# Kernel tuning notes

Hardware: AMD Instinct MI355X
Metric: run time of the kernel (lower is better)

The kernel has to match this reference:

```python
import jax, jax.numpy as jnp
import numpy as np

SEQ, IN, H = 64, 100000, 50


def setup_inputs() -> dict:
    key = jax.random.key(0)
    k0, k1, k2, k3, k4 = jax.random.split(key, 5)
    x = jax.random.normal(k0, (SEQ, 1, IN), dtype=jnp.float32) * 0.02
    Wi = jax.random.normal(k1, (IN, 4 * H), dtype=jnp.float32) * 0.01
    bi = jax.random.normal(k2, (4 * H,), dtype=jnp.float32) * 0.01
    Wh = jax.random.normal(k3, (H, 4 * H), dtype=jnp.float32) * 0.1
    bh = jax.random.normal(k4, (4 * H,), dtype=jnp.float32) * 0.01
    return {"x": x, "Wi": Wi, "bi": bi, "Wh": Wh, "bh": bh}


def reference(x, Wi, bi, Wh, bh):
    # x: [seq, batch=1, input_size] -- each row is a flattened ParameterList.
    # Precompute the input projection for all steps at once (one big GEMM),
    # same math as per-step input_weights(input) since it has no recurrence.
    gates_in = jnp.einsum('sbi,ig->sbg', x, Wi) + bi + bh  # [seq, 1, 4H]

    def step(carry, g_in):
        hx, cx = carry
        gates = g_in + hx @ Wh  # [1, 4H]
        i, f, g, o = jnp.split(gates, 4, axis=1)
        i = jax.nn.sigmoid(i)
        f = jax.nn.sigmoid(f)
        g = jnp.tanh(g)
        o = jax.nn.sigmoid(o)
        cy = f * cx + i * g
        hy = o * jnp.tanh(cy)
        return (hy, cy), None

    h0 = jnp.zeros((1, H), dtype=x.dtype)
    c0 = jnp.zeros((1, H), dtype=x.dtype)
    (h_final, _), _ = jax.lax.scan(step, (h0, c0), gates_in)
    # torch.squeeze(out_hidden): (1, H) -> (H,)
    return jnp.squeeze(h_final)
```

## Files before the change

kernel.cpp:

```cpp
#include <hip/hip_runtime.h>
#include <hip/hip_bf16.h>


#define K_DIM 100000
#define NG 200
#define NS 64
#define TK 32
#define NBLK 512
#define KSTRIDE (NBLK * TK)
#define CELLS (NS * NG)

__global__ __launch_bounds__(512, 4) void k1_gemm_partial(
    const float* __restrict__ x, const float* __restrict__ Wi,
    float* __restrict__ partial)
{
    __shared__ float4 ws4[TK * 50 + 16];

    const int tid  = threadIdx.x;
    const int lane = tid & 63;
    const int wave = tid >> 6;
    const int s0u  = __builtin_amdgcn_readfirstlane(wave * 8);

    float4 acc4[8];
#pragma unroll
    for (int j = 0; j < 8; ++j) acc4[j] = make_float4(0.f, 0.f, 0.f, 0.f);

    int kt = blockIdx.x * TK;
    const float4* wi4 = (const float4*)Wi;

    float4 w0, w1, w2, w3 = make_float4(0.f, 0.f, 0.f, 0.f);
    {
        const float4* wt = wi4 + (size_t)kt * 50;
        w0 = wt[tid];
        w1 = wt[tid + 512];
        w2 = wt[tid + 1024];
        if (tid < 64) w3 = wt[tid + 1536];
    }

    for (; kt < K_DIM; kt += KSTRIDE) {
        __syncthreads();
        ws4[tid]        = w0;
        ws4[tid + 512]  = w1;
        ws4[tid + 1024] = w2;
        if (tid < 64) ws4[tid + 1536] = w3;
        __syncthreads();

        int ktn = kt + KSTRIDE;
        if (ktn < K_DIM) {
            const float4* wt = wi4 + (size_t)ktn * 50;
            w0 = wt[tid];
            w1 = wt[tid + 512];
            w2 = wt[tid + 1024];
            if (tid < 64) w3 = wt[tid + 1536];
        }

        const float* xt = x + (size_t)s0u * K_DIM + kt;
        float4 xc[8], xn[8];
#pragma unroll
        for (int i = 0; i < 8; ++i)
            xc[i] = *(const float4*)(xt + (size_t)i * K_DIM);

#pragma unroll
        for (int k4 = 0; k4 < TK / 4; ++k4) {
            if (k4 + 1 < TK / 4) {
#pragma unroll
                for (int i = 0; i < 8; ++i)
                    xn[i] = *(const float4*)(xt + (size_t)i * K_DIM + (k4 + 1) * 4);
            }
#pragma unroll
            for (int kk = 0; kk < 4; ++kk) {
                float4 wv = ws4[(k4 * 4 + kk) * 50 + lane];
#pragma unroll
                for (int i = 0; i < 8; ++i) {
                    float xv = (kk == 0) ? xc[i].x : (kk == 1) ? xc[i].y
                             : (kk == 2) ? xc[i].z : xc[i].w;
                    acc4[i].x = fmaf(wv.x, xv, acc4[i].x);
                    acc4[i].y = fmaf(wv.y, xv, acc4[i].y);
                    acc4[i].z = fmaf(wv.z, xv, acc4[i].z);
                    acc4[i].w = fmaf(wv.w, xv, acc4[i].w);
                }
            }
            if (k4 + 1 < TK / 4) {
#pragma unroll
                for (int i = 0; i < 8; ++i) xc[i] = xn[i];
            }
        }
    }

    if (lane < 50) {
        float4* pout = (float4*)(partial + (size_t)blockIdx.x * CELLS) + lane;
#pragma unroll
        for (int si = 0; si < 8; ++si)
            pout[(s0u + si) * 50] = acc4[si];
    }
}

__global__ __launch_bounds__(512) void k2_reduce(
    const float* __restrict__ partial, const float* __restrict__ bi,
    const float* __restrict__ bh, float* __restrict__ gates)
{
    __shared__ float red[512];
    const int tid   = threadIdx.x;
    const int lane  = tid & 63;
    const int slice = tid >> 6;
    const int cell  = blockIdx.x * 64 + lane;

    float sum = 0.f;
#pragma unroll 8
    for (int b = slice * 64; b < (slice + 1) * 64; ++b)
        sum += partial[(size_t)b * CELLS + cell];
    red[tid] = sum;
    __syncthreads();
    if (slice == 0) {
        float tot = red[lane];
#pragma unroll
        for (int p = 1; p < 8; ++p) tot += red[p * 64 + lane];
        int g = cell % NG;
        gates[cell] = tot + bi[g] + bh[g];
    }
}

__global__ __launch_bounds__(256) void k3_lstm(
    const float* __restrict__ gates, const float* __restrict__ Wh,
    float* __restrict__ out)
{
    __shared__ float gz[CELLS];
    __shared__ float h_lds[64];
    __shared__ float act_lds[NG];
    const int g = threadIdx.x;

    for (int i = g; i < CELLS; i += 256) gz[i] = gates[i];

    float wh[50];
    if (g < NG) {
#pragma unroll
        for (int j = 0; j < 50; ++j) wh[j] = Wh[j * NG + g];
    }
    if (g < 64) h_lds[g] = 0.f;
    float c = 0.f, h = 0.f;
    const bool is_cell_gate = (g >= 100 && g < 150);
    __syncthreads();

    for (int s = 0; s < 64; ++s) {
        if (g < NG) {
            float a0 = gz[s * NG + g];
            float a1 = 0.f;
#pragma unroll
            for (int jj = 0; jj < 50; jj += 2) {
                float2 h2 = *(const float2*)(h_lds + jj);
                a0 = fmaf(h2.x, wh[jj],     a0);
                a1 = fmaf(h2.y, wh[jj + 1], a1);
            }
            float z = a0 + a1;
            float e   = __expf(-z);
            float sig = 1.f / (1.f + e);
            float e2  = e * e;
            float th  = (1.f - e2) / (1.f + e2);
            act_lds[g] = is_cell_gate ? th : sig;
        }
        __syncthreads();
        if (g < 50) {
            float iv = act_lds[g];
            float fv = act_lds[50 + g];
            float gv = act_lds[100 + g];
            float ov = act_lds[150 + g];
            c = fmaf(fv, c, iv * gv);
            float e2c = __expf(-2.f * c);
            h = ov * (1.f - e2c) / (1.f + e2c);
            h_lds[g] = h;
        }
        __syncthreads();
    }
    if (g < 50) out[g] = h;
}

extern "C" void kernel_launch(void* const* d_in, const int* in_sizes, int n_in,
                              void* d_out, int out_size, void* d_ws, size_t ws_size,
                              hipStream_t stream)
{
    const float* x  = (const float*)d_in[0];
    const float* Wi = (const float*)d_in[1];
    const float* bi = (const float*)d_in[2];
    const float* Wh = (const float*)d_in[3];
    const float* bh = (const float*)d_in[4];
    float* out = (float*)d_out;

    float* partial = (float*)d_ws;
    float* gates   = partial + (size_t)NBLK * CELLS;

    k1_gemm_partial<<<NBLK, 512, 0, stream>>>(x, Wi, partial);
    k2_reduce<<<CELLS / 64, 512, 0, stream>>>(partial, bi, bh, gates);
    k3_lstm<<<1, 256, 0, stream>>>(gates, Wh, out);
}
```

Baseline: 208.6 us.

## Distribute x loads across lanes with readlane broadcast, vectorize reduce and LSTM dot

In the GEMM kernel, each lane now loads one float4 of x per k-tile, and values are broadcast with readlane. Previously every lane issued identical uniform loads for 8 rows, so this cuts redundant x loads and register pressure, at the cost of many v_readlane instructions in the inner loop. The reduce kernel now uses float4 loads and a 32-way LDS tree. The LSTM recurrence dot product uses float4 LDS reads and four accumulators to shorten the dependency chain.

Result: no change. 207.8 us (-0.3%).

```diff
diff --git a/kernel.cpp b/kernel.cpp
--- a/kernel.cpp
+++ b/kernel.cpp
@@ -9,6 +9,11 @@
 #define NBLK 512
 #define KSTRIDE (NBLK * TK)
 #define CELLS (NS * NG)
+#define CELLS4 (CELLS / 4)
+
+static __device__ __forceinline__ float rl(float v, int l) {
+    return __int_as_float(__builtin_amdgcn_readlane(__float_as_int(v), l));
+}
 
 __global__ __launch_bounds__(512, 4) void k1_gemm_partial(
     const float* __restrict__ x, const float* __restrict__ Wi,
@@ -19,7 +24,11 @@
     const int tid  = threadIdx.x;
     const int lane = tid & 63;
     const int wave = tid >> 6;
-    const int s0u  = __builtin_amdgcn_readfirstlane(wave * 8);
+    const int s0   = wave * 8;
+
+    const int xrow  = s0 + (lane >> 3);
+    const int xkoff = (lane & 7) << 2;
+    const float* xbase = x + (size_t)xrow * K_DIM + xkoff;
 
     float4 acc4[8];
 #pragma unroll
@@ -28,13 +37,14 @@
     int kt = blockIdx.x * TK;
     const float4* wi4 = (const float4*)Wi;
 
-    float4 w0, w1, w2, w3 = make_float4(0.f, 0.f, 0.f, 0.f);
+    float4 w0, w1, w2, w3 = make_float4(0.f, 0.f, 0.f, 0.f), xc, xn;
     {
         const float4* wt = wi4 + (size_t)kt * 50;
         w0 = wt[tid];
         w1 = wt[tid + 512];
         w2 = wt[tid + 1024];
         if (tid < 64) w3 = wt[tid + 1536];
+        xc = *(const float4*)(xbase + kt);
     }
 
     for (; kt < K_DIM; kt += KSTRIDE) {
@@ -52,46 +62,34 @@
             w1 = wt[tid + 512];
             w2 = wt[tid + 1024];
             if (tid < 64) w3 = wt[tid + 1536];
-        }
-
-        const float* xt = x + (size_t)s0u * K_DIM + kt;
-        float4 xc[8], xn[8];
-#pragma unroll
-        for (int i = 0; i < 8; ++i)
-            xc[i] = *(const float4*)(xt + (size_t)i * K_DIM);
-
-#pragma unroll
-        for (int k4 = 0; k4 < TK / 4; ++k4) {
-            if (k4 + 1 < TK / 4) {
-#pragma unroll
-                for (int i = 0; i < 8; ++i)
-                    xn[i] = *(const float4*)(xt + (size_t)i * K_DIM + (k4 + 1) * 4);
-            }
+            xn = *(const float4*)(xbase + ktn);
+        }
+
+#pragma unroll
+        for (int q = 0; q < 8; ++q) {
 #pragma unroll
             for (int kk = 0; kk < 4; ++kk) {
-                float4 wv = ws4[(k4 * 4 + kk) * 50 + lane];
-#pragma unroll
-                for (int i = 0; i < 8; ++i) {
-                    float xv = (kk == 0) ? xc[i].x : (kk == 1) ? xc[i].y
-                             : (kk == 2) ? xc[i].z : xc[i].w;
-                    acc4[i].x = fmaf(wv.x, xv, acc4[i].x);
-                    acc4[i].y = fmaf(wv.y, xv, acc4[i].y);
-                    acc4[i].z = fmaf(wv.z, xv, acc4[i].z);
-                    acc4[i].w = fmaf(wv.w, xv, acc4[i].w);
+                float4 wv = ws4[(q * 4 + kk) * 50 + lane];
+                float xcomp = (kk == 0) ? xc.x : (kk == 1) ? xc.y
+                            : (kk == 2) ? xc.z : xc.w;
+#pragma unroll
+                for (int r = 0; r < 8; ++r) {
+                    float xv = rl(xcomp, r * 8 + q);
+                    acc4[r].x = fmaf(wv.x, xv, acc4[r].x);
+                    acc4[r].y = fmaf(wv.y, xv, acc4[r].y);
+                    acc4[r].z = fmaf(wv.z, xv, acc4[r].z);
+                    acc4[r].w = fmaf(wv.w, xv, acc4[r].w);
                 }
             }
-            if (k4 + 1 < TK / 4) {
-#pragma unroll
-                for (int i = 0; i < 8; ++i) xc[i] = xn[i];
-            }
-        }
+        }
+        xc = xn;
     }
 
     if (lane < 50) {
         float4* pout = (float4*)(partial + (size_t)blockIdx.x * CELLS) + lane;
 #pragma unroll
         for (int si = 0; si < 8; ++si)
-            pout[(s0u + si) * 50] = acc4[si];
+            pout[(s0 + si) * 50] = acc4[si];
     }
 }
 
@@ -99,24 +97,34 @@
     const float* __restrict__ partial, const float* __restrict__ bi,
     const float* __restrict__ bh, float* __restrict__ gates)
 {
-    __shared__ float red[512];
+    __shared__ float4 red[512];
     const int tid   = threadIdx.x;
-    const int lane  = tid & 63;
-    const int slice = tid >> 6;
-    const int cell  = blockIdx.x * 64 + lane;
-
-    float sum = 0.f;
-#pragma unroll 8
-    for (int b = slice * 64; b < (slice + 1) * 64; ++b)
-        sum += partial[(size_t)b * CELLS + cell];
+    const int fid   = tid & 15;
+    const int slice = tid >> 4;
+    const int g4    = blockIdx.x * 16 + fid;
+
+    const float4* p4 = (const float4*)partial;
+    float4 sum = make_float4(0.f, 0.f, 0.f, 0.f);
+#pragma unroll 4
+    for (int b = slice * 16; b < slice * 16 + 16; ++b) {
+        float4 v = p4[(size_t)b * CELLS4 + g4];
+        sum.x += v.x; sum.y += v.y; sum.z += v.z; sum.w += v.w;
+    }
     red[tid] = sum;
     __syncthreads();
-    if (slice == 0) {
-        float tot = red[lane];
-#pragma unroll
-        for (int p = 1; p < 8; ++p) tot += red[p * 64 + lane];
-        int g = cell % NG;
-        gates[cell] = tot + bi[g] + bh[g];
+    if (tid < 16) {
+        float4 tot = red[tid];
+#pragma unroll
+        for (int p = 1; p < 32; ++p) {
+            float4 v = red[p * 16 + tid];
+            tot.x += v.x; tot.y += v.y; tot.z += v.z; tot.w += v.w;
+        }
+        int gg = (g4 * 4) % NG;
+        float4 b1 = *(const float4*)(bi + gg);
+        float4 b2 = *(const float4*)(bh + gg);
+        tot.x += b1.x + b2.x; tot.y += b1.y + b2.y;
+        tot.z += b1.z + b2.z; tot.w += b1.w + b2.w;
+        ((float4*)gates)[g4] = tot;
     }
 }
 
@@ -143,15 +151,21 @@
 
     for (int s = 0; s < 64; ++s) {
         if (g < NG) {
-            float a0 = gz[s * NG + g];
-            float a1 = 0.f;
-#pragma unroll
-            for (int jj = 0; jj < 50; jj += 2) {
-                float2 h2 = *(const float2*)(h_lds + jj);
-                a0 = fmaf(h2.x, wh[jj],     a0);
-                a1 = fmaf(h2.y, wh[jj + 1], a1);
+            float a0 = gz[s * NG + g], a1 = 0.f, a2 = 0.f, a3 = 0.f;
+#pragma unroll
+            for (int jj = 0; jj < 48; jj += 4) {
+                float4 h4 = *(const float4*)(h_lds + jj);
+                a0 = fmaf(h4.x, wh[jj],     a0);
+                a1 = fmaf(h4.y, wh[jj + 1], a1);
+                a2 = fmaf(h4.z, wh[jj + 2], a2);
+                a3 = fmaf(h4.w, wh[jj + 3], a3);
             }
-            float z = a0 + a1;
+            {
+                float2 h2 = *(const float2*)(h_lds + 48);
+                a0 = fmaf(h2.x, wh[48], a0);
+                a1 = fmaf(h2.y, wh[49], a1);
+            }
+            float z = (a0 + a1) + (a2 + a3);
             float e   = __expf(-z);
             float sig = 1.f / (1.f + e);
             float e2  = e * e;
@@ -189,6 +203,6 @@
     float* gates   = partial + (size_t)NBLK * CELLS;
 
     k1_gemm_partial<<<NBLK, 512, 0, stream>>>(x, Wi, partial);
-    k2_reduce<<<CELLS / 64, 512, 0, stream>>>(partial, bi, bh, gates);
+    k2_reduce<<<CELLS4 / 16, 512, 0, stream>>>(partial, bi, bh, gates);
     k3_lstm<<<1, 256, 0, stream>>>(gates, Wh, out);
 }
```
